# Kernel optimization log

Hardware: AMD Instinct MI355X
Metric: run time of the kernel (lower is better)

The kernel has to match this reference:

```python
import jax, jax.numpy as jnp
import numpy as np

DIM = 1024
HEADS = 16
DIM_HEAD = 64
INNER = HEADS * DIM_HEAD  # 1024
MLP = 4096
NQ = 16384
NW = 1024
LN_EPS = 1e-5
L2_EPS = 1e-12


def setup_inputs() -> dict:
    key = jax.random.key(0)
    ks = jax.random.split(key, 12)
    s = 0.02
    return {
        "queries": jax.random.normal(ks[0], (NQ, DIM), jnp.float32),
        "prototypes": jax.random.normal(ks[1], (NW, DIM), jnp.float32),
        "ln1_w": 1.0 + s * jax.random.normal(ks[2], (DIM,), jnp.float32),
        "ln1_b": s * jax.random.normal(ks[3], (DIM,), jnp.float32),
        "wq": s * jax.random.normal(ks[4], (DIM, INNER), jnp.float32),
        "wk": s * jax.random.normal(ks[5], (DIM, INNER), jnp.float32),
        "wv": s * jax.random.normal(ks[6], (DIM, INNER), jnp.float32),
        "wo": s * jax.random.normal(ks[7], (INNER, DIM), jnp.float32),
        "bo": jnp.zeros((DIM,), jnp.float32),
        "ln2_w": 1.0 + s * jax.random.normal(ks[8], (DIM,), jnp.float32),
        "ln2_b": s * jax.random.normal(ks[9], (DIM,), jnp.float32),
        "w1": s * jax.random.normal(ks[10], (DIM, MLP), jnp.float32),
        "b1": jnp.zeros((MLP,), jnp.float32),
        "w2": s * jax.random.normal(ks[11], (MLP, DIM), jnp.float32),
        "b2": jnp.zeros((DIM,), jnp.float32),
    }


def _layernorm(x, w, b):
    mu = jnp.mean(x, axis=-1, keepdims=True)
    var = jnp.mean(jnp.square(x - mu), axis=-1, keepdims=True)
    return (x - mu) * jax.lax.rsqrt(var + LN_EPS) * w + b


def _l2norm(x):
    n = jnp.sqrt(jnp.sum(jnp.square(x), axis=-1, keepdims=True))
    return x / jnp.maximum(n, L2_EPS)


def reference(queries, prototypes, ln1_w, ln1_b, wq, wk, wv, wo, bo,
              ln2_w, ln2_b, w1, b1, w2, b2):
    residual = queries
    qn = _layernorm(queries, ln1_w, ln1_b)
    pn = _layernorm(prototypes, ln1_w, ln1_b)
    # projections -> (h, q, d) / (h, n, d)
    q = (qn @ wq).reshape(NQ, HEADS, DIM_HEAD).transpose(1, 0, 2)
    k = (pn @ wk).reshape(NW, HEADS, DIM_HEAD).transpose(1, 0, 2)
    v = (pn @ wv).reshape(NW, HEADS, DIM_HEAD).transpose(1, 0, 2)
    attn = jnp.einsum('hqd,hnd->hqn', _l2norm(q), _l2norm(k))  # cosine, no softmax
    out = jnp.einsum('hqn,hnd->hqd', attn, v)
    out = out.transpose(1, 0, 2).reshape(NQ, INNER)
    out = out @ wo + bo + residual
    residual2 = out
    h = _layernorm(out, ln2_w, ln2_b)
    h = jax.nn.gelu(h @ w1 + b1, approximate=False) @ w2 + b2
    return h + residual2
```

## Files before the change

kernel.cpp:

```cpp
#include <hip/hip_runtime.h>
#include <hip/hip_bf16.h>

typedef _Float16 f16;
typedef __attribute__((ext_vector_type(8))) _Float16 f16x8;
typedef __attribute__((ext_vector_type(4))) _Float16 f16x4;
typedef __attribute__((ext_vector_type(4))) float f32x4;

#define DIM 1024
#define HEADS 16
#define DHEAD 64
#define MLPD 4096
#define NQ 16384
#define NW 1024
#define MCHUNK 32

__device__ __forceinline__ void glds16(const f16* g, f16* l) {
  __builtin_amdgcn_global_load_lds(
      (const __attribute__((address_space(1))) void*)g,
      (__attribute__((address_space(3))) void*)l, 16, 0, 0);
}

__global__ __launch_bounds__(256) void ln_f16_k(
    const float* __restrict__ X, const float* __restrict__ w,
    const float* __restrict__ b, f16* __restrict__ O) {
  const int row = blockIdx.x;
  const int t = threadIdx.x;
  const float4 v = ((const float4*)(X + (long)row * DIM))[t];
  float s = v.x + v.y + v.z + v.w;
  float s2 = v.x * v.x + v.y * v.y + v.z * v.z + v.w * v.w;
#pragma unroll
  for (int m = 1; m < 64; m <<= 1) {
    s += __shfl_xor(s, m);
    s2 += __shfl_xor(s2, m);
  }
  __shared__ float ps[4], ps2[4];
  const int lane = t & 63, wid = t >> 6;
  if (lane == 0) { ps[wid] = s; ps2[wid] = s2; }
  __syncthreads();
  s = ps[0] + ps[1] + ps[2] + ps[3];
  s2 = ps2[0] + ps2[1] + ps2[2] + ps2[3];
  const float mu = s * (1.0f / DIM);
  const float inv = rsqrtf(s2 * (1.0f / DIM) - mu * mu + 1e-5f);
  const float4 wv = ((const float4*)w)[t];
  const float4 bv = ((const float4*)b)[t];
  f16x4 o;
  o[0] = (f16)((v.x - mu) * inv * wv.x + bv.x);
  o[1] = (f16)((v.y - mu) * inv * wv.y + bv.y);
  o[2] = (f16)((v.z - mu) * inv * wv.z + bv.z);
  o[3] = (f16)((v.w - mu) * inv * wv.w + bv.w);
  *(f16x4*)(O + (long)row * DIM + t * 4) = o;
}

__global__ __launch_bounds__(256) void tcast_k(const float* __restrict__ X,
                                               f16* __restrict__ O, int R, int C) {
  __shared__ float tile[32][33];
  const int c0 = blockIdx.x * 32, r0 = blockIdx.y * 32;
  const int tx = threadIdx.x, ty = threadIdx.y;
#pragma unroll
  for (int j = 0; j < 4; ++j)
    tile[ty + j * 8][tx] = X[(long)(r0 + ty + j * 8) * C + c0 + tx];
  __syncthreads();
#pragma unroll
  for (int j = 0; j < 4; ++j)
    O[(long)(c0 + ty + j * 8) * R + r0 + tx] = (f16)tile[tx][ty + j * 8];
}

__global__ __launch_bounds__(256) void calc_m_part_k(const f16* __restrict__ kh,
                                                     const f16* __restrict__ v,
                                                     float* __restrict__ Mp) {
  const int h = blockIdx.x, ch = blockIdx.y;
  const int t = threadIdx.x;
  const int d1 = t >> 2;
  const int d2b = (t & 3) * 16;
  float acc[16] = {};
  const int n0 = ch * (NW / MCHUNK);
#pragma unroll 4
  for (int n = n0; n < n0 + NW / MCHUNK; ++n) {
    const float kv = (float)kh[(long)n * DIM + h * DHEAD + d1];
    const f16x8* vp = (const f16x8*)&v[(long)n * DIM + h * DHEAD + d2b];
    const f16x8 v0 = vp[0], v1 = vp[1];
#pragma unroll
    for (int j = 0; j < 8; ++j) acc[j] += kv * (float)v0[j];
#pragma unroll
    for (int j = 0; j < 8; ++j) acc[8 + j] += kv * (float)v1[j];
  }
  float* o = &Mp[((long)(h * MCHUNK + ch)) * 4096 + d1 * 64 + d2b];
#pragma unroll
  for (int j = 0; j < 16; ++j) o[j] = acc[j];
}

__global__ __launch_bounds__(256) void calc_m_reduce_k(const float* __restrict__ Mp,
                                                       float* __restrict__ Mo) {
  const int h = blockIdx.x;
  const int t = threadIdx.x;
#pragma unroll
  for (int e = t; e < 4096; e += 256) {
    float s = 0.f;
#pragma unroll
    for (int c = 0; c < MCHUNK; ++c)
      s += Mp[((long)(h * MCHUNK + c)) * 4096 + e];
    Mo[h * 4096 + e] = s;
  }
}

__global__ __launch_bounds__(256) void calc_wefft_k(const float* __restrict__ M,
                                                    const float* __restrict__ wo,
                                                    f16* __restrict__ Wt) {
  const int h = blockIdx.x, jt = blockIdx.y;
  const int t = threadIdx.x;
  const int jl = t & 63;
  const int il0 = (t >> 6) * 16;
  const int j = jt * 64 + jl;
  float acc[16] = {};
  for (int d = 0; d < DHEAD; ++d) {
    const float w = wo[(long)(h * DHEAD + d) * DIM + j];
    const float* mrow = &M[h * 4096 + il0 * 64 + d];
#pragma unroll
    for (int r = 0; r < 16; ++r) acc[r] += mrow[r * 64] * w;
  }
#pragma unroll
  for (int r = 0; r < 16; ++r)
    Wt[(long)j * DIM + h * DHEAD + il0 + r] = (f16)acc[r];
}

enum {
  EPI_F16 = 0,
  EPI_L2N = 1,
  EPI_BIAS_RES = 2,
  EPI_GELU = 3
};

template <int EPI>
__global__ __launch_bounds__(512, 2) void gemm256(
    const f16* __restrict__ A, const f16* __restrict__ Bt, int M, int N, int K,
    const float* __restrict__ bias, const float* resid, void* out) {
  __shared__ __align__(16) f16 lds[65536];

  const int tid = threadIdx.x;
  const int lane = tid & 63;
  const int wid = tid >> 6;
  const int wm = wid >> 2;
  const int wn = wid & 3;
  const int l15 = lane & 15;

  int bm, bn;
  {
    const int orig = blockIdx.y * gridDim.x + blockIdx.x;
    if ((gridDim.x & 7) == 0) {
      const int slab = orig & 7;
      const int idx = orig >> 3;
      const int sm = gridDim.x >> 3;
      bm = slab * sm + idx % sm;
      bn = idx / sm;
    } else {
      bm = blockIdx.x;
      bn = blockIdx.y;
    }
  }

  const int scol8 = (((tid & 3) ^ ((tid >> 3) & 3))) * 8;
  const f16* aSrc = A + (long)(bm * 256 + (tid >> 2)) * K + scol8;
  const f16* bSrc = Bt + (long)(bn * 256 + (tid >> 2)) * K + scol8;
  const long hK = (long)128 * K;
  const int tid8 = tid * 8;

  const int rslot8 = (((lane >> 4) ^ ((l15 >> 1) & 3))) * 8;
  const int aRdBase = (wm * 128 + l15) * 32 + rslot8;
  const int bRdBase = 16384 + (wn * 64 + l15) * 32 + rslot8;

  f32x4 acc[8][4] = {};
  const int NT = K >> 6;

#define STAGE_A0(Ld, ko)                              \
  glds16(aSrc + (ko), (Ld) + tid8);                   \
  glds16(aSrc + hK + (ko), (Ld) + 4096 + tid8)
#define STAGE_A1(Ld, ko)                              \
  glds16(aSrc + (ko) + 32, (Ld) + 8192 + tid8);       \
  glds16(aSrc + hK + (ko) + 32, (Ld) + 8192 + 4096 + tid8)
#define STAGE_B0(Ld, ko)                              \
  glds16(bSrc + (ko), (Ld) + 16384 + tid8);           \
  glds16(bSrc + hK + (ko), (Ld) + 16384 + 4096 + tid8)
#define STAGE_B1(Ld, ko)                              \
  glds16(bSrc + (ko) + 32, (Ld) + 24576 + tid8);      \
  glds16(bSrc + hK + (ko) + 32, (Ld) + 24576 + 4096 + tid8)

#define BURST(AF, BF, MB)                                                 \
  __builtin_amdgcn_s_setprio(1);                                          \
  _Pragma("unroll") for (int j = 0; j < 4; ++j)                           \
      _Pragma("unroll") for (int nj = 0; nj < 4; ++nj)                    \
          acc[(MB) + j][nj] = __builtin_amdgcn_mfma_f32_16x16x32_f16(     \
              AF[j], BF[nj], acc[(MB) + j][nj], 0, 0, 0);                 \
  __builtin_amdgcn_s_setprio(0)

  STAGE_A0(lds, 0);
  STAGE_B0(lds, 0);
  STAGE_A1(lds, 0);
  STAGE_B1(lds, 0);
  __syncthreads();

  f16x8 bA[4], bB[4], aA[4], aB[4], aC[4], aD[4];
#pragma unroll
  for (int j = 0; j < 4; ++j) bA[j] = *(const f16x8*)&lds[bRdBase + j * 512];
#pragma unroll
  for (int j = 0; j < 4; ++j) aA[j] = *(const f16x8*)&lds[aRdBase + j * 512];

  for (int g = 0; g < NT; ++g) {
    f16* L = &lds[(g & 1) * 32768];
    f16* Lo = &lds[((g & 1) ^ 1) * 32768];
    const long ko1 = (long)(g + 1) * 64;
    const bool s1 = (g + 1) < NT;

    if (s1) { STAGE_A0(Lo, ko1); STAGE_B0(Lo, ko1); }
#pragma unroll
    for (int j = 0; j < 4; ++j)
      aB[j] = *(const f16x8*)&L[aRdBase + 2048 + j * 512];
    BURST(aA, bA, 0);
    if (s1) { STAGE_A1(Lo, ko1); STAGE_B1(Lo, ko1); }
#pragma unroll
    for (int j = 0; j < 4; ++j)
      bB[j] = *(const f16x8*)&L[8192 + bRdBase + j * 512];
#pragma unroll
    for (int j = 0; j < 4; ++j)
      aC[j] = *(const f16x8*)&L[8192 + aRdBase + j * 512];
    BURST(aB, bA, 4);
#pragma unroll
    for (int j = 0; j < 4; ++j)
      aD[j] = *(const f16x8*)&L[8192 + aRdBase + 2048 + j * 512];
    BURST(aC, bB, 0);
    BURST(aD, bB, 4);

    __syncthreads();
    if (s1) {
#pragma unroll
      for (int j = 0; j < 4; ++j) bA[j] = *(const f16x8*)&Lo[bRdBase + j * 512];
#pragma unroll
      for (int j = 0; j < 4; ++j) aA[j] = *(const f16x8*)&Lo[aRdBase + j * 512];
    }
  }
#undef STAGE_A0
#undef STAGE_A1
#undef STAGE_B0
#undef STAGE_B1
#undef BURST

  const int r0 = bm * 256 + wm * 128;
  const int c0 = bn * 256 + wn * 64;
  const int lr = (lane >> 4) * 4;
  const int lc = l15;

#pragma unroll
  for (int mi = 0; mi < 8; ++mi) {
#pragma unroll
    for (int i = 0; i < 4; ++i) {
      const long r = r0 + mi * 16 + lr + i;
      if (EPI == EPI_L2N) {
        float ss = 0.f;
#pragma unroll
        for (int nj = 0; nj < 4; ++nj) {
          const float x = acc[mi][nj][i];
          ss += x * x;
        }
        ss += __shfl_xor(ss, 1);
        ss += __shfl_xor(ss, 2);
        ss += __shfl_xor(ss, 4);
        ss += __shfl_xor(ss, 8);
        const float inv = 1.0f / fmaxf(sqrtf(ss), 1e-12f);
#pragma unroll
        for (int nj = 0; nj < 4; ++nj)
          ((f16*)out)[r * N + c0 + nj * 16 + lc] = (f16)(acc[mi][nj][i] * inv);
      } else if (EPI == EPI_F16) {
#pragma unroll
        for (int nj = 0; nj < 4; ++nj)
          ((f16*)out)[r * N + c0 + nj * 16 + lc] = (f16)acc[mi][nj][i];
      } else if (EPI == EPI_BIAS_RES) {
#pragma unroll
        for (int nj = 0; nj < 4; ++nj) {
          const long c = c0 + nj * 16 + lc;
          ((float*)out)[r * N + c] = acc[mi][nj][i] + bias[c] + resid[r * N + c];
        }
      } else {
#pragma unroll
        for (int nj = 0; nj < 4; ++nj) {
          const long c = c0 + nj * 16 + lc;
          const float x = acc[mi][nj][i] + bias[c];
          const float u = 0.7978845608028654f * (x + 0.044715f * x * x * x);
          const float z = __expf(fminf(-2.0f * u, 88.0f));
          const float th = (1.0f - z) / (1.0f + z);
          ((f16*)out)[r * N + c] = (f16)(0.5f * x * (1.0f + th));
        }
      }
    }
  }
}

extern "C" void kernel_launch(void* const* d_in, const int* in_sizes, int n_in,
                              void* d_out, int out_size, void* d_ws, size_t ws_size,
                              hipStream_t stream) {
  (void)in_sizes; (void)n_in; (void)out_size;
  const float* queries = (const float*)d_in[0];
  const float* prototypes = (const float*)d_in[1];
  const float* ln1_w = (const float*)d_in[2];
  const float* ln1_b = (const float*)d_in[3];
  const float* wq = (const float*)d_in[4];
  const float* wk = (const float*)d_in[5];
  const float* wv = (const float*)d_in[6];
  const float* wo = (const float*)d_in[7];
  const float* bo = (const float*)d_in[8];
  const float* ln2_w = (const float*)d_in[9];
  const float* ln2_b = (const float*)d_in[10];
  const float* w1 = (const float*)d_in[11];
  const float* b1 = (const float*)d_in[12];
  const float* w2 = (const float*)d_in[13];
  const float* b2 = (const float*)d_in[14];

  char* ws = (char*)d_ws;
  const size_t MB = 1024ull * 1024ull;
  if (ws_size < 176ull * MB) return;

  f16* QN = (f16*)(ws + 0);
  f16* QHAT = (f16*)(ws + 32 * MB);
  f16* PN = (f16*)(ws + 64 * MB);
  f16* WQT = (f16*)(ws + 66 * MB);
  f16* WKT = (f16*)(ws + 68 * MB);
  f16* WVT = (f16*)(ws + 70 * MB);
  f16* KHAT = (f16*)(ws + 72 * MB);
  f16* VBF = (f16*)(ws + 74 * MB);
  float* Mbuf = (float*)(ws + 76 * MB);
  f16* WEFFT = (f16*)(ws + 77 * MB);
  float* Mpart = (float*)(ws + 0);
  f16* G = (f16*)(ws + 0);
  f16* HBF = (f16*)(ws + 128 * MB);
  f16* W1T = (f16*)(ws + 160 * MB);
  f16* W2T = (f16*)(ws + 168 * MB);
  float* RES2 = (float*)d_out;

  ln_f16_k<<<NQ, 256, 0, stream>>>(queries, ln1_w, ln1_b, QN);
  ln_f16_k<<<NW, 256, 0, stream>>>(prototypes, ln1_w, ln1_b, PN);
  tcast_k<<<dim3(32, 32), dim3(32, 8), 0, stream>>>(wq, WQT, DIM, DIM);
  tcast_k<<<dim3(32, 32), dim3(32, 8), 0, stream>>>(wk, WKT, DIM, DIM);
  tcast_k<<<dim3(32, 32), dim3(32, 8), 0, stream>>>(wv, WVT, DIM, DIM);
  tcast_k<<<dim3(128, 32), dim3(32, 8), 0, stream>>>(w1, W1T, DIM, MLPD);
  tcast_k<<<dim3(32, 128), dim3(32, 8), 0, stream>>>(w2, W2T, MLPD, DIM);

  gemm256<EPI_L2N><<<dim3(NQ / 256, DIM / 256), 512, 0, stream>>>(
      QN, WQT, NQ, DIM, DIM, nullptr, nullptr, QHAT);
  gemm256<EPI_L2N><<<dim3(NW / 256, DIM / 256), 512, 0, stream>>>(
      PN, WKT, NW, DIM, DIM, nullptr, nullptr, KHAT);
  gemm256<EPI_F16><<<dim3(NW / 256, DIM / 256), 512, 0, stream>>>(
      PN, WVT, NW, DIM, DIM, nullptr, nullptr, VBF);

  calc_m_part_k<<<dim3(HEADS, MCHUNK), 256, 0, stream>>>(KHAT, VBF, Mpart);
  calc_m_reduce_k<<<HEADS, 256, 0, stream>>>(Mpart, Mbuf);
  calc_wefft_k<<<dim3(HEADS, 16), 256, 0, stream>>>(Mbuf, wo, WEFFT);

  gemm256<EPI_BIAS_RES><<<dim3(NQ / 256, DIM / 256), 512, 0, stream>>>(
      QHAT, WEFFT, NQ, DIM, DIM, bo, queries, RES2);

  ln_f16_k<<<NQ, 256, 0, stream>>>(RES2, ln2_w, ln2_b, HBF);

  gemm256<EPI_GELU><<<dim3(NQ / 256, MLPD / 256), 512, 0, stream>>>(
      HBF, W1T, NQ, MLPD, DIM, b1, nullptr, G);
  gemm256<EPI_BIAS_RES><<<dim3(NQ / 256, DIM / 256), 512, 0, stream>>>(
      G, W2T, NQ, DIM, MLPD, b2, RES2, (float*)d_out);
}
```

Baseline: 636.4 us.

## Use triple-buffered K=32 GEMM pipeline and merge prologue kernels

The GEMM main loop moves from a double-buffered K=64 stage to a three-slot ring of K=32 stages. Loads are issued two iterations ahead and gated with explicit vmcnt waits and a raw s_barrier, and odd and even waves alternate the order of their A-fragment halves. The layernorm-1 launches and the five weight transpose-cast launches are each merged into one kernel to cut launch overhead. Nontemporal stores are used for the GELU and final outputs. The shallower K step means more barriers per tile, and the hand-written wait counts add correctness risk.

```diff
diff --git a/kernel.cpp b/kernel.cpp
--- a/kernel.cpp
+++ b/kernel.cpp
@@ -14,18 +14,19 @@
 #define NW 1024
 #define MCHUNK 32
 
+#define WAITV(n) asm volatile("s_waitcnt vmcnt(" #n ")" ::: "memory")
+
 __device__ __forceinline__ void glds16(const f16* g, f16* l) {
   __builtin_amdgcn_global_load_lds(
       (const __attribute__((address_space(1))) void*)g,
       (__attribute__((address_space(3))) void*)l, 16, 0, 0);
 }
 
-__global__ __launch_bounds__(256) void ln_f16_k(
-    const float* __restrict__ X, const float* __restrict__ w,
-    const float* __restrict__ b, f16* __restrict__ O) {
-  const int row = blockIdx.x;
-  const int t = threadIdx.x;
-  const float4 v = ((const float4*)(X + (long)row * DIM))[t];
+__device__ __forceinline__ void ln_body(const float* __restrict__ X,
+                                        const float* __restrict__ w,
+                                        const float* __restrict__ b,
+                                        f16* __restrict__ O, int t) {
+  const float4 v = ((const float4*)X)[t];
   float s = v.x + v.y + v.z + v.w;
   float s2 = v.x * v.x + v.y * v.y + v.z * v.z + v.w * v.w;
 #pragma unroll
@@ -48,21 +49,58 @@
   o[1] = (f16)((v.y - mu) * inv * wv.y + bv.y);
   o[2] = (f16)((v.z - mu) * inv * wv.z + bv.z);
   o[3] = (f16)((v.w - mu) * inv * wv.w + bv.w);
-  *(f16x4*)(O + (long)row * DIM + t * 4) = o;
-}
-
-__global__ __launch_bounds__(256) void tcast_k(const float* __restrict__ X,
-                                               f16* __restrict__ O, int R, int C) {
+  *(f16x4*)(O + t * 4) = o;
+}
+
+__global__ __launch_bounds__(256) void ln_f16_k(
+    const float* __restrict__ X, const float* __restrict__ w,
+    const float* __restrict__ b, f16* __restrict__ O) {
+  const long row = blockIdx.x;
+  ln_body(X + row * DIM, w, b, O + row * DIM, threadIdx.x);
+}
+
+__global__ __launch_bounds__(256) void ln1_all_k(
+    const float* __restrict__ q, const float* __restrict__ p,
+    const float* __restrict__ w, const float* __restrict__ b,
+    f16* __restrict__ QN, f16* __restrict__ PN) {
+  const long row = blockIdx.x;
+  if (row < NQ)
+    ln_body(q + row * DIM, w, b, QN + row * DIM, threadIdx.x);
+  else
+    ln_body(p + (row - NQ) * DIM, w, b, PN + (row - NQ) * DIM, threadIdx.x);
+}
+
+__global__ __launch_bounds__(256) void tcast_all_k(
+    const float* __restrict__ wq, const float* __restrict__ wk,
+    const float* __restrict__ wv, const float* __restrict__ w1,
+    const float* __restrict__ w2, f16* WQT, f16* WKT, f16* WVT, f16* W1T,
+    f16* W2T) {
+  const int id = blockIdx.x;
+  const float* X;
+  f16* O;
+  int R, C, tx, ty;
+  if (id < 3072) {
+    const int which = id >> 10, l = id & 1023;
+    X = which == 0 ? wq : which == 1 ? wk : wv;
+    O = which == 0 ? WQT : which == 1 ? WKT : WVT;
+    R = 1024; C = 1024; tx = l & 31; ty = l >> 5;
+  } else if (id < 7168) {
+    const int l = id - 3072;
+    X = w1; O = W1T; R = 1024; C = 4096; tx = l & 127; ty = l >> 7;
+  } else {
+    const int l = id - 7168;
+    X = w2; O = W2T; R = 4096; C = 1024; tx = l & 31; ty = l >> 5;
+  }
   __shared__ float tile[32][33];
-  const int c0 = blockIdx.x * 32, r0 = blockIdx.y * 32;
-  const int tx = threadIdx.x, ty = threadIdx.y;
+  const int c0 = tx * 32, r0 = ty * 32;
+  const int x = threadIdx.x, y = threadIdx.y;
 #pragma unroll
   for (int j = 0; j < 4; ++j)
-    tile[ty + j * 8][tx] = X[(long)(r0 + ty + j * 8) * C + c0 + tx];
+    tile[y + j * 8][x] = X[(long)(r0 + y + j * 8) * C + c0 + x];
   __syncthreads();
 #pragma unroll
   for (int j = 0; j < 4; ++j)
-    O[(long)(c0 + ty + j * 8) * R + r0 + tx] = (f16)tile[tx][ty + j * 8];
+    O[(long)(c0 + y + j * 8) * R + r0 + x] = (f16)tile[x][y + j * 8];
 }
 
 __global__ __launch_bounds__(256) void calc_m_part_k(const f16* __restrict__ kh,
@@ -127,14 +165,15 @@
   EPI_F16 = 0,
   EPI_L2N = 1,
   EPI_BIAS_RES = 2,
-  EPI_GELU = 3
+  EPI_GELU = 3,
+  EPI_OUT = 4
 };
 
 template <int EPI>
 __global__ __launch_bounds__(512, 2) void gemm256(
     const f16* __restrict__ A, const f16* __restrict__ Bt, int M, int N, int K,
     const float* __restrict__ bias, const float* resid, void* out) {
-  __shared__ __align__(16) f16 lds[65536];
+  __shared__ __align__(16) f16 lds[49152];
 
   const int tid = threadIdx.x;
   const int lane = tid & 63;
@@ -166,23 +205,18 @@
 
   const int rslot8 = (((lane >> 4) ^ ((l15 >> 1) & 3))) * 8;
   const int aRdBase = (wm * 128 + l15) * 32 + rslot8;
-  const int bRdBase = 16384 + (wn * 64 + l15) * 32 + rslot8;
+  const int bRdBase = 8192 + (wn * 64 + l15) * 32 + rslot8;
 
   f32x4 acc[8][4] = {};
-  const int NT = K >> 6;
-
-#define STAGE_A0(Ld, ko)                              \
-  glds16(aSrc + (ko), (Ld) + tid8);                   \
-  glds16(aSrc + hK + (ko), (Ld) + 4096 + tid8)
-#define STAGE_A1(Ld, ko)                              \
-  glds16(aSrc + (ko) + 32, (Ld) + 8192 + tid8);       \
-  glds16(aSrc + hK + (ko) + 32, (Ld) + 8192 + 4096 + tid8)
-#define STAGE_B0(Ld, ko)                              \
-  glds16(bSrc + (ko), (Ld) + 16384 + tid8);           \
-  glds16(bSrc + hK + (ko), (Ld) + 16384 + 4096 + tid8)
-#define STAGE_B1(Ld, ko)                              \
-  glds16(bSrc + (ko) + 32, (Ld) + 24576 + tid8);      \
-  glds16(bSrc + hK + (ko) + 32, (Ld) + 24576 + 4096 + tid8)
+  const int NT = K >> 5;
+
+  auto STAGE = [&](f16* Ld, int t) {
+    const long ko = (long)t * 32;
+    glds16(aSrc + ko, Ld + tid8);
+    glds16(aSrc + hK + ko, Ld + 4096 + tid8);
+    glds16(bSrc + ko, Ld + 8192 + tid8);
+    glds16(bSrc + hK + ko, Ld + 12288 + tid8);
+  };
 
 #define BURST(AF, BF, MB)                                                 \
   __builtin_amdgcn_s_setprio(1);                                          \
@@ -192,55 +226,47 @@
               AF[j], BF[nj], acc[(MB) + j][nj], 0, 0, 0);                 \
   __builtin_amdgcn_s_setprio(0)
 
-  STAGE_A0(lds, 0);
-  STAGE_B0(lds, 0);
-  STAGE_A1(lds, 0);
-  STAGE_B1(lds, 0);
-  __syncthreads();
-
-  f16x8 bA[4], bB[4], aA[4], aB[4], aC[4], aD[4];
-#pragma unroll
-  for (int j = 0; j < 4; ++j) bA[j] = *(const f16x8*)&lds[bRdBase + j * 512];
-#pragma unroll
-  for (int j = 0; j < 4; ++j) aA[j] = *(const f16x8*)&lds[aRdBase + j * 512];
-
+  STAGE(&lds[0], 0);
+  STAGE(&lds[16384], 1);
+  WAITV(4);
+  __builtin_amdgcn_s_barrier();
+  __builtin_amdgcn_sched_barrier(0);
+
+  const int worder = __builtin_amdgcn_readfirstlane(wid) & 1;
+  int c = 0;
   for (int g = 0; g < NT; ++g) {
-    f16* L = &lds[(g & 1) * 32768];
-    f16* Lo = &lds[((g & 1) ^ 1) * 32768];
-    const long ko1 = (long)(g + 1) * 64;
-    const bool s1 = (g + 1) < NT;
-
-    if (s1) { STAGE_A0(Lo, ko1); STAGE_B0(Lo, ko1); }
-#pragma unroll
-    for (int j = 0; j < 4; ++j)
-      aB[j] = *(const f16x8*)&L[aRdBase + 2048 + j * 512];
-    BURST(aA, bA, 0);
-    if (s1) { STAGE_A1(Lo, ko1); STAGE_B1(Lo, ko1); }
-#pragma unroll
-    for (int j = 0; j < 4; ++j)
-      bB[j] = *(const f16x8*)&L[8192 + bRdBase + j * 512];
-#pragma unroll
-    for (int j = 0; j < 4; ++j)
-      aC[j] = *(const f16x8*)&L[8192 + aRdBase + j * 512];
-    BURST(aB, bA, 4);
-#pragma unroll
-    for (int j = 0; j < 4; ++j)
-      aD[j] = *(const f16x8*)&L[8192 + aRdBase + 2048 + j * 512];
-    BURST(aC, bB, 0);
-    BURST(aD, bB, 4);
-
-    __syncthreads();
-    if (s1) {
-#pragma unroll
-      for (int j = 0; j < 4; ++j) bA[j] = *(const f16x8*)&Lo[bRdBase + j * 512];
-#pragma unroll
-      for (int j = 0; j < 4; ++j) aA[j] = *(const f16x8*)&Lo[aRdBase + j * 512];
+    const int cs = (c + 2 >= 3) ? c - 1 : c + 2;
+    if (g + 2 < NT) STAGE(&lds[cs * 16384], g + 2);
+
+    const f16* L = &lds[c * 16384];
+    f16x8 aA[4], aB[4], bA[4];
+#pragma unroll
+    for (int j = 0; j < 4; ++j) bA[j] = *(const f16x8*)&L[bRdBase + j * 512];
+    if (worder == 0) {
+#pragma unroll
+      for (int j = 0; j < 4; ++j) aA[j] = *(const f16x8*)&L[aRdBase + j * 512];
+      BURST(aA, bA, 0);
+#pragma unroll
+      for (int j = 0; j < 4; ++j)
+        aB[j] = *(const f16x8*)&L[aRdBase + 2048 + j * 512];
+      BURST(aB, bA, 4);
+    } else {
+#pragma unroll
+      for (int j = 0; j < 4; ++j)
+        aB[j] = *(const f16x8*)&L[aRdBase + 2048 + j * 512];
+      BURST(aB, bA, 4);
+#pragma unroll
+      for (int j = 0; j < 4; ++j) aA[j] = *(const f16x8*)&L[aRdBase + j * 512];
+      BURST(aA, bA, 0);
     }
-  }
-#undef STAGE_A0
-#undef STAGE_A1
-#undef STAGE_B0
-#undef STAGE_B1
+
+    if (g + 1 < NT) {
+      if (g + 2 < NT) { WAITV(4); } else { WAITV(0); }
+      __builtin_amdgcn_s_barrier();
+      __builtin_amdgcn_sched_barrier(0);
+    }
+    c = (c + 1 == 3) ? 0 : c + 1;
+  }
 #undef BURST
 
   const int r0 = bm * 256 + wm * 128;
@@ -275,18 +301,26 @@
       } else if (EPI == EPI_BIAS_RES) {
 #pragma unroll
         for (int nj = 0; nj < 4; ++nj) {
-          const long c = c0 + nj * 16 + lc;
-          ((float*)out)[r * N + c] = acc[mi][nj][i] + bias[c] + resid[r * N + c];
+          const long c2 = c0 + nj * 16 + lc;
+          ((float*)out)[r * N + c2] = acc[mi][nj][i] + bias[c2] + resid[r * N + c2];
         }
-      } else {
+      } else if (EPI == EPI_GELU) {
 #pragma unroll
         for (int nj = 0; nj < 4; ++nj) {
-          const long c = c0 + nj * 16 + lc;
-          const float x = acc[mi][nj][i] + bias[c];
+          const long c2 = c0 + nj * 16 + lc;
+          const float x = acc[mi][nj][i] + bias[c2];
           const float u = 0.7978845608028654f * (x + 0.044715f * x * x * x);
           const float z = __expf(fminf(-2.0f * u, 88.0f));
           const float th = (1.0f - z) / (1.0f + z);
-          ((f16*)out)[r * N + c] = (f16)(0.5f * x * (1.0f + th));
+          __builtin_nontemporal_store((f16)(0.5f * x * (1.0f + th)),
+                                      (f16*)out + r * N + c2);
+        }
+      } else {
+#pragma unroll
+        for (int nj = 0; nj < 4; ++nj) {
+          const long c2 = c0 + nj * 16 + lc;
+          const float v = acc[mi][nj][i] + bias[c2] + resid[r * N + c2];
+          __builtin_nontemporal_store(v, (float*)out + r * N + c2);
         }
       }
     }
@@ -334,13 +368,9 @@
   f16* W2T = (f16*)(ws + 168 * MB);
   float* RES2 = (float*)d_out;
 
-  ln_f16_k<<<NQ, 256, 0, stream>>>(queries, ln1_w, ln1_b, QN);
-  ln_f16_k<<<NW, 256, 0, stream>>>(prototypes, ln1_w, ln1_b, PN);
-  tcast_k<<<dim3(32, 32), dim3(32, 8), 0, stream>>>(wq, WQT, DIM, DIM);
-  tcast_k<<<dim3(32, 32), dim3(32, 8), 0, stream>>>(wk, WKT, DIM, DIM);
-  tcast_k<<<dim3(32, 32), dim3(32, 8), 0, stream>>>(wv, WVT, DIM, DIM);
-  tcast_k<<<dim3(128, 32), dim3(32, 8), 0, stream>>>(w1, W1T, DIM, MLPD);
-  tcast_k<<<dim3(32, 128), dim3(32, 8), 0, stream>>>(w2, W2T, MLPD, DIM);
+  ln1_all_k<<<NQ + NW, 256, 0, stream>>>(queries, prototypes, ln1_w, ln1_b, QN, PN);
+  tcast_all_k<<<11264, dim3(32, 8), 0, stream>>>(wq, wk, wv, w1, w2, WQT, WKT,
+                                                 WVT, W1T, W2T);
 
   gemm256<EPI_L2N><<<dim3(NQ / 256, DIM / 256), 512, 0, stream>>>(
       QN, WQT, NQ, DIM, DIM, nullptr, nullptr, QHAT);
@@ -360,6 +390,6 @@
 
   gemm256<EPI_GELU><<<dim3(NQ / 256, MLPD / 256), 512, 0, stream>>>(
       HBF, W1T, NQ, MLPD, DIM, b1, nullptr, G);
-  gemm256<EPI_BIAS_RES><<<dim3(NQ / 256, DIM / 256), 512, 0, stream>>>(
+  gemm256<EPI_OUT><<<dim3(NQ / 256, DIM / 256), 512, 0, stream>>>(
       G, W2T, NQ, DIM, MLPD, b2, RES2, (float*)d_out);
 }
```

After: 2.344 ms. 268% more time.
